# Optimization experiments

Measured on AMD Instinct MI355X. Metric: run time of the kernel, lower is better.

## Reference

```python
import jax, jax.numpy as jnp
import numpy as np

K = 2
N_NODES = 100_000
N_EDGES = 1_600_000
STATIC_F = 16
DYN_F = 32
EDGE_F = 8
IN_F = EDGE_F + 2 * STATIC_F + 2 * DYN_F  # 104
HID_F = 2 * DYN_F  # 64


def setup_inputs() -> dict:
    key = jax.random.key(0)
    ks = jax.random.split(key, 9)
    x_s = jax.random.normal(ks[0], (N_NODES, STATIC_F), dtype=jnp.float32)
    x_t = jax.random.normal(ks[1], (N_NODES, DYN_F), dtype=jnp.float32)
    edge_index = jax.random.randint(ks[2], (2, N_EDGES), 0, N_NODES, dtype=jnp.int64 if jax.config.jax_enable_x64 else jnp.int32)
    edge_attr = jax.random.normal(ks[3], (N_EDGES, EDGE_F), dtype=jnp.float32)
    W1 = jax.random.normal(ks[4], (IN_F, HID_F), dtype=jnp.float32) / np.sqrt(IN_F)
    b1 = jnp.zeros((HID_F,), dtype=jnp.float32)
    W2 = jax.random.normal(ks[5], (HID_F, DYN_F), dtype=jnp.float32) / np.sqrt(HID_F)
    b2 = jnp.zeros((DYN_F,), dtype=jnp.float32)
    F = jax.random.normal(ks[6], (K + 1, DYN_F, DYN_F), dtype=jnp.float32) / np.sqrt(DYN_F)
    return {"x_s": x_s, "x_t": x_t, "edge_index": edge_index, "edge_attr": edge_attr,
            "W1": W1, "b1": b1, "W2": W2, "b2": b2, "F": F}


def reference(x_s, x_t, edge_index, edge_attr, W1, b1, W2, b2, F):
    row, col = edge_index[0], edge_index[1]
    num_nodes = x_t.shape[0]
    # filter_matrix[0] (Linear, no bias); F[k] stored as [in, out]
    out = x_t @ F[0]
    xs_row = x_s[row]  # static gathers are loop-invariant
    xs_col = x_s[col]
    for k in range(K):
        mask = jnp.sum(out, axis=1) != 0  # [N]
        edge_mask = (mask[row] | mask[col]).astype(out.dtype)[:, None]  # [E,1]
        out_row = out[row]
        out_col = out[col]
        e_ij = jnp.concatenate([xs_row, xs_col, out_row, out_col, edge_attr], axis=1)  # [E,104]
        w_ij = jax.nn.relu(e_ij @ W1 + b1) @ W2 + b2  # [E,32]
        # normalize per edge; NaN (zero-norm) -> 0, matching masked_fill_
        nrm = jnp.linalg.norm(w_ij, axis=1, keepdims=True)
        w_ij = jnp.where(nrm > 0, w_ij / jnp.where(nrm > 0, nrm, 1.0), 0.0)
        # with_gradient: (x_j - x_i) * w_ij; zero out edges failing the mask
        shift = (out_col - out_row) * w_ij * edge_mask
        scattered = jax.ops.segment_sum(shift, col, num_segments=num_nodes)
        out = out + scattered @ F[k + 1]
    return out
```

## Files before the change

kernel.cpp:

```cpp
#include <hip/hip_runtime.h>

#define NN 100000
#define NE 1600000
#define SF 16
#define DF 32
#define EFT 8
#define HF 64

typedef __attribute__((ext_vector_type(8))) _Float16 half8;
typedef __attribute__((ext_vector_type(4))) _Float16 half4v;
typedef __attribute__((ext_vector_type(8))) short short8;
typedef __attribute__((ext_vector_type(4))) float floatx4;

__device__ inline int hswz(int row, int halfoff) {
  int gran = halfoff >> 3, sub = halfoff & 7;
  return row * 64 + ((gran ^ (row & 7)) << 3) + sub;
}

__global__ __launch_bounds__(256) void hist_kernel(const int* __restrict__ ei,
                                                   int* __restrict__ deg) {
  int e = blockIdx.x * 256 + threadIdx.x;
  if (e < NE) atomicAdd(&deg[ei[NE + e]], 1);
}

__global__ __launch_bounds__(256) void scan1_kernel(const int* __restrict__ deg,
                                                    int* __restrict__ cur,
                                                    int* __restrict__ bsums) {
  __shared__ int ts[256];
  int tid = threadIdx.x;
  int base = blockIdx.x * 1024 + tid * 4;
  int v[4];
#pragma unroll
  for (int q = 0; q < 4; ++q) v[q] = (base + q < NN) ? deg[base + q] : 0;
  int s = v[0] + v[1] + v[2] + v[3];
  ts[tid] = s;
  __syncthreads();
  for (int off = 1; off < 256; off <<= 1) {
    int t = (tid >= off) ? ts[tid - off] : 0;
    __syncthreads();
    ts[tid] += t;
    __syncthreads();
  }
  int excl = ts[tid] - s;
  if (tid == 255) bsums[blockIdx.x] = ts[255];
  int run = excl;
#pragma unroll
  for (int q = 0; q < 4; ++q) {
    if (base + q < NN) cur[base + q] = run;
    run += v[q];
  }
}

__global__ __launch_bounds__(256) void scan3_kernel(int* __restrict__ cur,
                                                    const int* __restrict__ bsums) {
  int i = blockIdx.x * 256 + threadIdx.x;
  int g = blockIdx.x >> 2;
  int pref = 0;
  for (int q = 0; q < g; ++q) pref += bsums[q];
  if (i < NN) cur[i] += pref;
}

__global__ __launch_bounds__(256) void setup_kernel(
    const float* __restrict__ W1, const float* __restrict__ W2,
    _Float16* __restrict__ WpreT, _Float16* __restrict__ w2pk,
    _Float16* __restrict__ w1epk,
    float4* __restrict__ scattered4, int* __restrict__ deg) {
  int gid = blockIdx.x * 256 + threadIdx.x;
  if (gid < 800000) {
    float4 z = {0.f, 0.f, 0.f, 0.f};
    scattered4[gid] = z;
  }
  if (gid < NN) deg[gid] = 0;
  if (gid < 128 * 64) {
    int col = gid >> 6, k = gid & 63;
    int j = col & 63;
    bool bh = col >= 64;
    float v = 0.f;
    if (k < 16) v = W1[((bh ? 16 : 0) + k) * HF + j];
    else if (k < 48) v = W1[((bh ? 64 : 32) + (k - 16)) * HF + j];
    WpreT[gid] = (_Float16)v;
  }
  if (gid < 2048) {
    int lane = gid >> 5, idx = gid & 31;
    int kt = idx >> 4, nt = (idx >> 3) & 1, q = idx & 7;
    int kgrp = (lane >> 4) & 3, lcol = lane & 15;
    w2pk[gid] = (_Float16)W2[(kt * 32 + kgrp * 8 + q) * DF + nt * 16 + lcol];
  } else if (gid < 4096) {
    int id = gid - 2048;
    int lane = id >> 5, idx = id & 31;
    int jblk = idx >> 3, t = idx & 7;
    float v = (lane < 16) ? W1[(96 + t) * HF + jblk * 16 + lane] : 0.f;
    w1epk[id] = (_Float16)v;
  }
}

__global__ __launch_bounds__(256) void fill_kernel(
    const int* __restrict__ ei, const float* __restrict__ ea,
    int* __restrict__ cur, char* __restrict__ recs) {
  int e = blockIdx.x * 256 + threadIdx.x;
  int r = ei[e];
  int c = ei[NE + e];
  int pos = atomicAdd(&cur[c], 1);
  const float4* p = (const float4*)(ea + (size_t)e * EFT);
  float4 v0 = p[0], v1 = p[1];
  union { _Float16 h[2]; int i; } p01, p23, p45, p67;
  p01.h[0] = (_Float16)v0.x; p01.h[1] = (_Float16)v0.y;
  p23.h[0] = (_Float16)v0.z; p23.h[1] = (_Float16)v0.w;
  p45.h[0] = (_Float16)v1.x; p45.h[1] = (_Float16)v1.y;
  p67.h[0] = (_Float16)v1.z; p67.h[1] = (_Float16)v1.w;
  int2* rp = (int2*)(recs + (size_t)pos * 24);
  int2 a = {r, c};
  int2 b = {p01.i, p23.i};
  int2 d = {p45.i, p67.i};
  rp[0] = a; rp[1] = b; rp[2] = d;
}

__global__ __launch_bounds__(256) void init_kernel(
    const float* __restrict__ x_t, const float* __restrict__ F0,
    float* __restrict__ out, _Float16* __restrict__ outb,
    float* __restrict__ sums) {
  int n = blockIdx.x * 256 + threadIdx.x;
  if (n >= NN) return;
  float x[DF];
  const float4* xr = reinterpret_cast<const float4*>(x_t + (size_t)n * DF);
#pragma unroll
  for (int q = 0; q < 8; ++q) {
    float4 v = xr[q];
    x[4*q+0]=v.x; x[4*q+1]=v.y; x[4*q+2]=v.z; x[4*q+3]=v.w;
  }
  float4* orow = reinterpret_cast<float4*>(out + (size_t)n * DF);
  _Float16* ob = outb + (size_t)n * DF;
  float s = 0.f;
#pragma unroll
  for (int q = 0; q < 8; ++q) {
    float4 acc = {0.f, 0.f, 0.f, 0.f};
#pragma unroll
    for (int i = 0; i < DF; ++i) {
      float xi = x[i];
      acc.x = fmaf(xi, F0[i*DF + 4*q+0], acc.x);
      acc.y = fmaf(xi, F0[i*DF + 4*q+1], acc.y);
      acc.z = fmaf(xi, F0[i*DF + 4*q+2], acc.z);
      acc.w = fmaf(xi, F0[i*DF + 4*q+3], acc.w);
    }
    orow[q] = acc;
    s += acc.x + acc.y + acc.z + acc.w;
    half4v pk = {(_Float16)acc.x, (_Float16)acc.y, (_Float16)acc.z, (_Float16)acc.w};
    *(half4v*)(ob + 4*q) = pk;
  }
  sums[n] = s;
}

__global__ __launch_bounds__(256, 4) void pre_kernel(
    const float* __restrict__ x_s, const _Float16* __restrict__ outb,
    const _Float16* __restrict__ WpreT, _Float16* __restrict__ ABh) {
  __shared__ _Float16 wlds[128][72];
  __shared__ _Float16 st[64][136];
  int tid = threadIdx.x;
  for (int t = tid; t < 1024; t += 256) {
    int colr = t >> 3, kc = t & 7;
    *(half8*)(&wlds[colr][kc * 8]) = *(const half8*)(WpreT + colr * 64 + kc * 8);
  }
  __syncthreads();

  int lcol = tid & 15, kgrp = (tid >> 4) & 3, wid = tid >> 6;
  int nodebase = blockIdx.x * 64 + wid * 16;
  int nodeA = nodebase + lcol;

  half8 a0 = {}, a1 = {};
  if (nodeA < NN) {
    const _Float16* obp = outb + (size_t)nodeA * DF;
    if (kgrp < 2) {
      const float4* p = (const float4*)(x_s + (size_t)nodeA * SF);
      float4 v0 = p[kgrp * 2], v1 = p[kgrp * 2 + 1];
      a0[0]=(_Float16)v0.x; a0[1]=(_Float16)v0.y;
      a0[2]=(_Float16)v0.z; a0[3]=(_Float16)v0.w;
      a0[4]=(_Float16)v1.x; a0[5]=(_Float16)v1.y;
      a0[6]=(_Float16)v1.z; a0[7]=(_Float16)v1.w;
      a1 = *(const half8*)(obp + 16 + kgrp * 8);
    } else if (kgrp == 2) {
      a0 = *(const half8*)(obp + 0);
    } else {
      a0 = *(const half8*)(obp + 8);
    }
  }

  floatx4 acc[8];
#pragma unroll
  for (int nt = 0; nt < 8; ++nt) {
    half8 b0 = *(const half8*)(&wlds[nt * 16 + lcol][kgrp * 8]);
    half8 b1v = *(const half8*)(&wlds[nt * 16 + lcol][32 + kgrp * 8]);
    floatx4 c = {0.f, 0.f, 0.f, 0.f};
    c = __builtin_amdgcn_mfma_f32_16x16x32_f16(a0, b0, c, 0, 0, 0);
    c = __builtin_amdgcn_mfma_f32_16x16x32_f16(a1, b1v, c, 0, 0, 0);
    acc[nt] = c;
  }

#pragma unroll
  for (int nt = 0; nt < 8; ++nt) {
#pragma unroll
    for (int rr = 0; rr < 4; ++rr)
      st[wid * 16 + kgrp * 4 + rr][nt * 16 + lcol] = (_Float16)acc[nt][rr];
  }
  int nl = tid >> 2, q = tid & 3;
  int node = blockIdx.x * 64 + nl;
  if (node < NN) {
    _Float16* dst = ABh + (size_t)node * 128 + q * 32;
#pragma unroll
    for (int s = 0; s < 4; ++s)
      *(half8*)(dst + s * 8) = *(const half8*)(&st[nl][q * 32 + s * 8]);
  }
}

__global__ __launch_bounds__(256, 4) void edge_kernel(
    const _Float16* __restrict__ ABh, const _Float16* __restrict__ outb,
    const float* __restrict__ sums, const char* __restrict__ recs,
    const float* __restrict__ b1, const float* __restrict__ b2,
    const _Float16* __restrict__ w2pk, const _Float16* __restrict__ w1epk,
    float* __restrict__ scattered) {
  __shared__ union { _Float16 h[256 * 64]; float sh[256 * 33]; } u;
  __shared__ int scol[256];
  __shared__ unsigned short l0[256], l1[256];
  __shared__ int wbase[4];
  __shared__ int cnt;

  int tid = threadIdx.x;
  int bid;
  {
    int xcd = blockIdx.x & 7, idx = blockIdx.x >> 3;
    const int qq = 781, rrem = 2;
    bid = (xcd < rrem) ? xcd * (qq + 1) + idx
                       : rrem * (qq + 1) + (xcd - rrem) * qq + idx;
  }
  int bbase = bid * 256;
  int i = bbase + tid;
  if (tid == 0) cnt = 0;
  int lcol = tid & 15, kgrp = (tid >> 4) & 3, wid = tid >> 6;
  int lane = tid & 63;

  const int2* rp = (const int2*)(recs + (size_t)i * 24);
  int2 ra = rp[0], rb = rp[1], rd = rp[2];
  int r = ra.x;
  int c = ra.y;
  int4 eai = {rb.x, rb.y, rd.x, rd.y};
  scol[tid] = c;
  float s_r = sums[r], s_c = sums[c];

  half8 Ar[8], Bc[8];
  {
    const half8* arp = (const half8*)(ABh + (size_t)r * 128);
    const half8* bcp = (const half8*)(ABh + (size_t)c * 128 + 64);
#pragma unroll
    for (int q = 0; q < 8; ++q) { Ar[q] = arp[q]; Bc[q] = bcp[q]; }
  }

  float b2c0 = b2[lcol], b2c1 = b2[16 + lcol];

  const _Float16* wep = w1epk + (size_t)lane * 32;
  half8 wA0 = *(const half8*)(wep);
  half8 wA1 = *(const half8*)(wep + 8);
  half8 wA2 = *(const half8*)(wep + 16);
  half8 wA3 = *(const half8*)(wep + 24);
  const float4* b1f4 = (const float4*)b1;
  float4 b1q0 = b1f4[0 + kgrp];
  float4 b1q1 = b1f4[4 + kgrp];
  float4 b1q2 = b1f4[8 + kgrp];
  float4 b1q3 = b1f4[12 + kgrp];
  bool lo16 = lane < 16;
#pragma unroll
  for (int g = 0; g < 4; ++g) {
    int src = g * 16 + lcol;
    int4 t;
    t.x = __shfl(eai.x, src, 64);
    t.y = __shfl(eai.y, src, 64);
    t.z = __shfl(eai.z, src, 64);
    t.w = __shfl(eai.w, src, 64);
    half8 zz = {};
    half8 bg = lo16 ? __builtin_bit_cast(half8, t) : zz;
    int erow = wid * 64 + g * 16 + lcol;
    {
      floatx4 cc = {b1q0.x, b1q0.y, b1q0.z, b1q0.w};
      cc = __builtin_amdgcn_mfma_f32_16x16x32_f16(wA0, bg, cc, 0, 0, 0);
      half4v h4 = {(_Float16)cc[0], (_Float16)cc[1], (_Float16)cc[2], (_Float16)cc[3]};
      *(half4v*)(&u.h[hswz(erow, 0 * 16 + kgrp * 4)]) = h4;
    }
    {
      floatx4 cc = {b1q1.x, b1q1.y, b1q1.z, b1q1.w};
      cc = __builtin_amdgcn_mfma_f32_16x16x32_f16(wA1, bg, cc, 0, 0, 0);
      half4v h4 = {(_Float16)cc[0], (_Float16)cc[1], (_Float16)cc[2], (_Float16)cc[3]};
      *(half4v*)(&u.h[hswz(erow, 1 * 16 + kgrp * 4)]) = h4;
    }
    {
      floatx4 cc = {b1q2.x, b1q2.y, b1q2.z, b1q2.w};
      cc = __builtin_amdgcn_mfma_f32_16x16x32_f16(wA2, bg, cc, 0, 0, 0);
      half4v h4 = {(_Float16)cc[0], (_Float16)cc[1], (_Float16)cc[2], (_Float16)cc[3]};
      *(half4v*)(&u.h[hswz(erow, 2 * 16 + kgrp * 4)]) = h4;
    }
    {
      floatx4 cc = {b1q3.x, b1q3.y, b1q3.z, b1q3.w};
      cc = __builtin_amdgcn_mfma_f32_16x16x32_f16(wA3, bg, cc, 0, 0, 0);
      half4v h4 = {(_Float16)cc[0], (_Float16)cc[1], (_Float16)cc[2], (_Float16)cc[3]};
      *(half4v*)(&u.h[hswz(erow, 3 * 16 + kgrp * 4)]) = h4;
    }
  }

#pragma unroll
  for (int q = 0; q < 8; ++q) {
    int idx = hswz(tid, q * 8);
    half8 w = *(const half8*)(&u.h[idx]);
    half8 s = Ar[q] + Bc[q] + w;
    short8 sb = __builtin_bit_cast(short8, s);
    short8 m = sb >> 15;
    sb = sb & ~m;
    *(short8*)(&u.h[idx]) = sb;
  }

  const _Float16* wpp = w2pk + (size_t)lane * 32;
  half8 w2f00 = *(const half8*)(wpp);
  half8 w2f01 = *(const half8*)(wpp + 8);
  half8 w2f10 = *(const half8*)(wpp + 16);
  half8 w2f11 = *(const half8*)(wpp + 24);
  floatx4 acc[4][2];
#pragma unroll
  for (int g = 0; g < 4; ++g) {
    int erow = wid * 64 + g * 16 + lcol;
    half8 a0 = *(const half8*)(&u.h[hswz(erow, kgrp * 8)]);
    half8 a1 = *(const half8*)(&u.h[hswz(erow, 32 + kgrp * 8)]);
    floatx4 c0 = {b2c0, b2c0, b2c0, b2c0};
    floatx4 c1 = {b2c1, b2c1, b2c1, b2c1};
    c0 = __builtin_amdgcn_mfma_f32_16x16x32_f16(a0, w2f00, c0, 0, 0, 0);
    c0 = __builtin_amdgcn_mfma_f32_16x16x32_f16(a1, w2f10, c0, 0, 0, 0);
    c1 = __builtin_amdgcn_mfma_f32_16x16x32_f16(a0, w2f01, c1, 0, 0, 0);
    c1 = __builtin_amdgcn_mfma_f32_16x16x32_f16(a1, w2f11, c1, 0, 0, 0);
    acc[g][0] = c0;
    acc[g][1] = c1;
  }

  half8 Or[4], Oc[4];
  {
    const half8* orp = (const half8*)(outb + (size_t)r * DF);
    const half8* ocp = (const half8*)(outb + (size_t)c * DF);
#pragma unroll
    for (int q = 0; q < 4; ++q) { Or[q] = orp[q]; Oc[q] = ocp[q]; }
  }

  __syncthreads();

#pragma unroll
  for (int g = 0; g < 4; ++g) {
#pragma unroll
    for (int rr = 0; rr < 4; ++rr) {
      int e = wid * 64 + g * 16 + kgrp * 4 + rr;
      u.sh[e * 33 + lcol]      = acc[g][0][rr];
      u.sh[e * 33 + 16 + lcol] = acc[g][1][rr];
    }
  }

  {
    float o2[32];
    float nsq = 0.f;
#pragma unroll
    for (int j = 0; j < 32; ++j) {
      float v = u.sh[tid * 33 + j];
      o2[j] = v;
      nsq = fmaf(v, v, nsq);
    }
    float ms = (nsq > 0.f) ? rsqrtf(nsq) : 0.f;
    if (s_r == 0.f && s_c == 0.f) ms = 0.f;
#pragma unroll
    for (int q = 0; q < 4; ++q) {
#pragma unroll
      for (int jj = 0; jj < 8; ++jj)
        u.sh[tid * 33 + q * 8 + jj] =
            ((float)Oc[q][jj] - (float)Or[q][jj]) * o2[q * 8 + jj] * ms;
    }
  }
  __syncthreads();

  int c_self = scol[tid];
  bool head = (tid == 0 || scol[tid - 1] != c_self);
  unsigned long long m = __ballot(head);
  if (lane == 0) wbase[wid] = atomicAdd(&cnt, (int)__popcll(m));
  __syncthreads();
  if (head) {
    int idx = wbase[wid] + (int)__popcll(m & ((1ull << lane) - 1ull));
    int t1 = tid + 1;
    while (t1 < 256 && scol[t1] == c_self) ++t1;
    l0[idx] = (unsigned short)tid;
    l1[idx] = (unsigned short)t1;
  }
  __syncthreads();
  int nr = cnt;
  for (int task = tid; task < nr * 32; task += 256) {
    int rid = task >> 5, j = task & 31;
    int t0 = l0[rid], t1 = l1[rid];
    float s = 0.f;
    for (int t = t0; t < t1; ++t) s += u.sh[t * 33 + j];
    unsafeAtomicAdd(&scattered[(size_t)scol[t0] * DF + j], s);
  }
}

__global__ __launch_bounds__(256) void node_kernel(
    float* __restrict__ out, float* __restrict__ scattered,
    const float* __restrict__ Fk, _Float16* __restrict__ outb,
    float* __restrict__ sums) {
  int n = blockIdx.x * 256 + threadIdx.x;
  if (n >= NN) return;
  float s[DF];
  float4* sp = reinterpret_cast<float4*>(scattered + (size_t)n * DF);
#pragma unroll
  for (int q = 0; q < 8; ++q) {
    float4 v = sp[q];
    s[4*q+0]=v.x; s[4*q+1]=v.y; s[4*q+2]=v.z; s[4*q+3]=v.w;
  }
  float4* op = reinterpret_cast<float4*>(out + (size_t)n * DF);
  _Float16* ob = outb + (size_t)n * DF;
  float ssum = 0.f;
#pragma unroll
  for (int q = 0; q < 8; ++q) {
    float4 acc = op[q];
#pragma unroll
    for (int i = 0; i < DF; ++i) {
      float si = s[i];
      acc.x = fmaf(si, Fk[i*DF + 4*q+0], acc.x);
      acc.y = fmaf(si, Fk[i*DF + 4*q+1], acc.y);
      acc.z = fmaf(si, Fk[i*DF + 4*q+2], acc.z);
      acc.w = fmaf(si, Fk[i*DF + 4*q+3], acc.w);
    }
    op[q] = acc;
    ssum += acc.x + acc.y + acc.z + acc.w;
    half4v pk = {(_Float16)acc.x, (_Float16)acc.y, (_Float16)acc.z, (_Float16)acc.w};
    *(half4v*)(ob + 4*q) = pk;
  }
  sums[n] = ssum;
  float4 z = {0.f, 0.f, 0.f, 0.f};
#pragma unroll
  for (int q = 0; q < 8; ++q) sp[q] = z;
}

extern "C" void kernel_launch(void* const* d_in, const int* in_sizes, int n_in,
                              void* d_out, int out_size, void* d_ws, size_t ws_size,
                              hipStream_t stream) {
  const float* x_s = (const float*)d_in[0];
  const float* x_t = (const float*)d_in[1];
  const int*   ei  = (const int*)d_in[2];
  const float* ea  = (const float*)d_in[3];
  const float* W1  = (const float*)d_in[4];
  const float* b1  = (const float*)d_in[5];
  const float* W2  = (const float*)d_in[6];
  const float* b2  = (const float*)d_in[7];
  const float* F   = (const float*)d_in[8];

  float* out = (float*)d_out;
  char* ws = (char*)d_ws;
  float*     scattered = (float*)(ws);
  _Float16*  ABh       = (_Float16*)(ws + 12800000);
  _Float16*  outb      = (_Float16*)(ws + 38400000);
  float*     sums      = (float*)(ws + 44800000);
  char*      recs      = (char*)(ws + 45200000);
  int*       deg       = (int*)(ws + 83600000);
  int*       cur       = (int*)(ws + 84000000);
  int*       bsums     = (int*)(ws + 84400000);
  _Float16*  WpreT     = (_Float16*)(ws + 84410000);
  _Float16*  w2pk      = (_Float16*)(ws + 84430000);
  _Float16*  w1epk     = (_Float16*)(ws + 84440000);

  dim3 blk(256);
  dim3 grid_e(NE / 256);
  dim3 grid_n((NN + 255) / 256);
  dim3 grid_p((NN + 63) / 64);
  int nscan = (NN + 1023) / 1024;

  setup_kernel<<<3125, blk, 0, stream>>>(W1, W2, WpreT, w2pk, w1epk,
                                         (float4*)scattered, deg);
  hist_kernel<<<grid_e, blk, 0, stream>>>(ei, deg);
  scan1_kernel<<<nscan, blk, 0, stream>>>(deg, cur, bsums);
  scan3_kernel<<<grid_n, blk, 0, stream>>>(cur, bsums);
  fill_kernel<<<grid_e, blk, 0, stream>>>(ei, ea, cur, recs);

  init_kernel<<<grid_n, blk, 0, stream>>>(x_t, F, out, outb, sums);

  for (int k = 0; k < 2; ++k) {
    pre_kernel<<<grid_p, blk, 0, stream>>>(x_s, outb, WpreT, ABh);
    edge_kernel<<<grid_e, blk, 0, stream>>>(ABh, outb, sums, recs, b1, b2,
                                            w2pk, w1epk, scattered);
    node_kernel<<<grid_n, blk, 0, stream>>>(out, scattered,
                                            F + (size_t)(k + 1) * DF * DF,
                                            outb, sums);
  }
}
```

Baseline: 449.1 us.

## Shrink edge kernel LDS via fp8 hidden staging and fp16 shifts, raise occupancy

Stores the first-layer hidden activations in LDS as fp8 (converted back to fp16 for MFMA) and the per-edge shift vectors as fp16 instead of fp32. This shrinks the shared buffer from about 33KB to about 18KB so launch bounds can request 8 blocks per SM. It also drops the XCD-aware block remapping and one barrier. It trades precision of the hidden layer and shift values for higher occupancy, and adds conversion instructions.

```diff
diff --git a/kernel.cpp b/kernel.cpp
--- a/kernel.cpp
+++ b/kernel.cpp
@@ -9,12 +9,35 @@
 
 typedef __attribute__((ext_vector_type(8))) _Float16 half8;
 typedef __attribute__((ext_vector_type(4))) _Float16 half4v;
+typedef __attribute__((ext_vector_type(2))) _Float16 half2v;
+typedef __attribute__((ext_vector_type(2))) __fp16 fp16x2;
 typedef __attribute__((ext_vector_type(8))) short short8;
 typedef __attribute__((ext_vector_type(4))) float floatx4;
-
-__device__ inline int hswz(int row, int halfoff) {
-  int gran = halfoff >> 3, sub = halfoff & 7;
-  return row * 64 + ((gran ^ (row & 7)) << 3) + sub;
+typedef __attribute__((ext_vector_type(2))) float floatx2;
+
+__device__ inline half2v pkrtz2(float a, float b) {
+  fp16x2 t = __builtin_amdgcn_cvt_pkrtz(a, b);
+  return __builtin_bit_cast(half2v, t);
+}
+
+__device__ inline unsigned int pk_fp8x4(float a, float b, float c, float d) {
+  int v = __builtin_amdgcn_cvt_pk_fp8_f32(a, b, 0, false);
+  v = __builtin_amdgcn_cvt_pk_fp8_f32(c, d, v, true);
+  return (unsigned int)v;
+}
+__device__ inline half8 oct2h8(uint2 w) {
+  floatx2 a = __builtin_amdgcn_cvt_pk_f32_fp8((int)w.x, false);
+  floatx2 b = __builtin_amdgcn_cvt_pk_f32_fp8((int)w.x, true);
+  floatx2 c = __builtin_amdgcn_cvt_pk_f32_fp8((int)w.y, false);
+  floatx2 d = __builtin_amdgcn_cvt_pk_f32_fp8((int)w.y, true);
+  half2v p0 = pkrtz2(a[0], a[1]);
+  half2v p1 = pkrtz2(b[0], b[1]);
+  half2v p2 = pkrtz2(c[0], c[1]);
+  half2v p3 = pkrtz2(d[0], d[1]);
+  half8 r;
+  r[0]=p0[0]; r[1]=p0[1]; r[2]=p1[0]; r[3]=p1[1];
+  r[4]=p2[0]; r[5]=p2[1]; r[6]=p3[0]; r[7]=p3[1];
+  return r;
 }
 
 __global__ __launch_bounds__(256) void hist_kernel(const int* __restrict__ ei,
@@ -211,27 +234,23 @@
   }
 }
 
-__global__ __launch_bounds__(256, 4) void edge_kernel(
+__global__ __launch_bounds__(256, 8) void edge_kernel(
     const _Float16* __restrict__ ABh, const _Float16* __restrict__ outb,
     const float* __restrict__ sums, const char* __restrict__ recs,
     const float* __restrict__ b1, const float* __restrict__ b2,
     const _Float16* __restrict__ w2pk, const _Float16* __restrict__ w1epk,
     float* __restrict__ scattered) {
-  __shared__ union { _Float16 h[256 * 64]; float sh[256 * 33]; } u;
+  __shared__ unsigned short lds[256 * 36];
   __shared__ int scol[256];
-  __shared__ unsigned short l0[256], l1[256];
+  __shared__ unsigned char l0[256], lenm1[256];
   __shared__ int wbase[4];
   __shared__ int cnt;
 
+  unsigned char* hb = (unsigned char*)lds;
+  _Float16* shh = (_Float16*)lds;
+
   int tid = threadIdx.x;
-  int bid;
-  {
-    int xcd = blockIdx.x & 7, idx = blockIdx.x >> 3;
-    const int qq = 781, rrem = 2;
-    bid = (xcd < rrem) ? xcd * (qq + 1) + idx
-                       : rrem * (qq + 1) + (xcd - rrem) * qq + idx;
-  }
-  int bbase = bid * 256;
+  int bbase = blockIdx.x * 256;
   int i = bbase + tid;
   if (tid == 0) cnt = 0;
   int lcol = tid & 15, kgrp = (tid >> 4) & 3, wid = tid >> 6;
@@ -277,41 +296,43 @@
     half8 zz = {};
     half8 bg = lo16 ? __builtin_bit_cast(half8, t) : zz;
     int erow = wid * 64 + g * 16 + lcol;
+    unsigned char* hrow = hb + erow * 72 + kgrp * 4;
     {
       floatx4 cc = {b1q0.x, b1q0.y, b1q0.z, b1q0.w};
       cc = __builtin_amdgcn_mfma_f32_16x16x32_f16(wA0, bg, cc, 0, 0, 0);
-      half4v h4 = {(_Float16)cc[0], (_Float16)cc[1], (_Float16)cc[2], (_Float16)cc[3]};
-      *(half4v*)(&u.h[hswz(erow, 0 * 16 + kgrp * 4)]) = h4;
+      *(unsigned int*)(hrow + 0)  = pk_fp8x4(cc[0], cc[1], cc[2], cc[3]);
     }
     {
       floatx4 cc = {b1q1.x, b1q1.y, b1q1.z, b1q1.w};
       cc = __builtin_amdgcn_mfma_f32_16x16x32_f16(wA1, bg, cc, 0, 0, 0);
-      half4v h4 = {(_Float16)cc[0], (_Float16)cc[1], (_Float16)cc[2], (_Float16)cc[3]};
-      *(half4v*)(&u.h[hswz(erow, 1 * 16 + kgrp * 4)]) = h4;
+      *(unsigned int*)(hrow + 16) = pk_fp8x4(cc[0], cc[1], cc[2], cc[3]);
     }
     {
       floatx4 cc = {b1q2.x, b1q2.y, b1q2.z, b1q2.w};
       cc = __builtin_amdgcn_mfma_f32_16x16x32_f16(wA2, bg, cc, 0, 0, 0);
-      half4v h4 = {(_Float16)cc[0], (_Float16)cc[1], (_Float16)cc[2], (_Float16)cc[3]};
-      *(half4v*)(&u.h[hswz(erow, 2 * 16 + kgrp * 4)]) = h4;
+      *(unsigned int*)(hrow + 32) = pk_fp8x4(cc[0], cc[1], cc[2], cc[3]);
     }
     {
       floatx4 cc = {b1q3.x, b1q3.y, b1q3.z, b1q3.w};
       cc = __builtin_amdgcn_mfma_f32_16x16x32_f16(wA3, bg, cc, 0, 0, 0);
-      half4v h4 = {(_Float16)cc[0], (_Float16)cc[1], (_Float16)cc[2], (_Float16)cc[3]};
-      *(half4v*)(&u.h[hswz(erow, 3 * 16 + kgrp * 4)]) = h4;
+      *(unsigned int*)(hrow + 48) = pk_fp8x4(cc[0], cc[1], cc[2], cc[3]);
     }
   }
 
 #pragma unroll
   for (int q = 0; q < 8; ++q) {
-    int idx = hswz(tid, q * 8);
-    half8 w = *(const half8*)(&u.h[idx]);
-    half8 s = Ar[q] + Bc[q] + w;
+    unsigned char* p = hb + tid * 72 + q * 8;
+    uint2 w = *(const uint2*)p;
+    half8 wf = oct2h8(w);
+    half8 s = Ar[q] + Bc[q] + wf;
     short8 sb = __builtin_bit_cast(short8, s);
     short8 m = sb >> 15;
     sb = sb & ~m;
-    *(short8*)(&u.h[idx]) = sb;
+    half8 sr = __builtin_bit_cast(half8, sb);
+    uint2 o;
+    o.x = pk_fp8x4((float)sr[0], (float)sr[1], (float)sr[2], (float)sr[3]);
+    o.y = pk_fp8x4((float)sr[4], (float)sr[5], (float)sr[6], (float)sr[7]);
+    *(uint2*)p = o;
   }
 
   const _Float16* wpp = w2pk + (size_t)lane * 32;
@@ -323,8 +344,9 @@
 #pragma unroll
   for (int g = 0; g < 4; ++g) {
     int erow = wid * 64 + g * 16 + lcol;
-    half8 a0 = *(const half8*)(&u.h[hswz(erow, kgrp * 8)]);
-    half8 a1 = *(const half8*)(&u.h[hswz(erow, 32 + kgrp * 8)]);
+    const unsigned char* hr = hb + erow * 72;
+    half8 a0 = oct2h8(*(const uint2*)(hr + kgrp * 8));
+    half8 a1 = oct2h8(*(const uint2*)(hr + 32 + kgrp * 8));
     floatx4 c0 = {b2c0, b2c0, b2c0, b2c0};
     floatx4 c1 = {b2c1, b2c1, b2c1, b2c1};
     c0 = __builtin_amdgcn_mfma_f32_16x16x32_f16(a0, w2f00, c0, 0, 0, 0);
@@ -343,15 +365,13 @@
     for (int q = 0; q < 4; ++q) { Or[q] = orp[q]; Oc[q] = ocp[q]; }
   }
 
-  __syncthreads();
-
 #pragma unroll
   for (int g = 0; g < 4; ++g) {
 #pragma unroll
     for (int rr = 0; rr < 4; ++rr) {
       int e = wid * 64 + g * 16 + kgrp * 4 + rr;
-      u.sh[e * 33 + lcol]      = acc[g][0][rr];
-      u.sh[e * 33 + 16 + lcol] = acc[g][1][rr];
+      shh[e * 36 + lcol]      = (_Float16)acc[g][0][rr];
+      shh[e * 36 + 16 + lcol] = (_Float16)acc[g][1][rr];
     }
   }
 
@@ -359,19 +379,31 @@
     float o2[32];
     float nsq = 0.f;
 #pragma unroll
-    for (int j = 0; j < 32; ++j) {
-      float v = u.sh[tid * 33 + j];
-      o2[j] = v;
-      nsq = fmaf(v, v, nsq);
+    for (int m = 0; m < 8; ++m) {
+      uint2 w = *(const uint2*)(hb + tid * 72 + m * 8);
+      half4v hv = __builtin_bit_cast(half4v, w);
+#pragma unroll
+      for (int jj = 0; jj < 4; ++jj) {
+        float v = (float)hv[jj];
+        o2[m * 4 + jj] = v;
+        nsq = fmaf(v, v, nsq);
+      }
     }
     float ms = (nsq > 0.f) ? rsqrtf(nsq) : 0.f;
     if (s_r == 0.f && s_c == 0.f) ms = 0.f;
 #pragma unroll
-    for (int q = 0; q < 4; ++q) {
-#pragma unroll
-      for (int jj = 0; jj < 8; ++jj)
-        u.sh[tid * 33 + q * 8 + jj] =
-            ((float)Oc[q][jj] - (float)Or[q][jj]) * o2[q * 8 + jj] * ms;
+    for (int m = 0; m < 8; ++m) {
+      int q = m >> 1, base = (m & 1) * 4;
+      float f0 = ((float)Oc[q][base+0] - (float)Or[q][base+0]) * o2[m*4+0] * ms;
+      float f1 = ((float)Oc[q][base+1] - (float)Or[q][base+1]) * o2[m*4+1] * ms;
+      float f2 = ((float)Oc[q][base+2] - (float)Or[q][base+2]) * o2[m*4+2] * ms;
+      float f3 = ((float)Oc[q][base+3] - (float)Or[q][base+3]) * o2[m*4+3] * ms;
+      half2v p0 = pkrtz2(f0, f1);
+      half2v p1 = pkrtz2(f2, f3);
+      uint2 o;
+      o.x = __builtin_bit_cast(unsigned int, p0);
+      o.y = __builtin_bit_cast(unsigned int, p1);
+      *(uint2*)(hb + tid * 72 + m * 8) = o;
     }
   }
   __syncthreads();
@@ -385,16 +417,17 @@
     int idx = wbase[wid] + (int)__popcll(m & ((1ull << lane) - 1ull));
     int t1 = tid + 1;
     while (t1 < 256 && scol[t1] == c_self) ++t1;
-    l0[idx] = (unsigned short)tid;
-    l1[idx] = (unsigned short)t1;
+    l0[idx] = (unsigned char)tid;
+    lenm1[idx] = (unsigned char)(t1 - tid - 1);
   }
   __syncthreads();
   int nr = cnt;
   for (int task = tid; task < nr * 32; task += 256) {
     int rid = task >> 5, j = task & 31;
-    int t0 = l0[rid], t1 = l1[rid];
+    int t0 = l0[rid];
+    int t1 = t0 + lenm1[rid] + 1;
     float s = 0.f;
-    for (int t = t0; t < t1; ++t) s += u.sh[t * 33 + j];
+    for (int t = t0; t < t1; ++t) s += (float)shh[t * 36 + j];
     unsafeAtomicAdd(&scattered[(size_t)scol[t0] * DF + j], s);
   }
 }
```

Measured after the change: 603.2 us. 34.3% more time.
